# Performance work log

Measured on AMD Instinct MI355X. Metric: run time of the kernel, lower is better.

Reference implementation:

```python
import jax, jax.numpy as jnp
import numpy as np

N_NODES = 100000
N_EDGES = 1600000
N_FEAT = 32
HIDDEN = 128
N_GRAPHS = 256
NUM_LAYERS = 2
LN_EPS = 1e-5


def setup_inputs() -> dict:
    key = jax.random.key(0)
    ks = jax.random.split(key, 10)
    x = jax.random.normal(ks[0], (N_NODES, N_FEAT), dtype=jnp.float32)
    edge_index = jax.random.randint(ks[1], (2, N_EDGES), 0, N_NODES, dtype=jnp.int64)
    batch_operator = jnp.sort(jax.random.randint(ks[2], (N_NODES,), 0, N_GRAPHS, dtype=jnp.int64))
    s_in = 1.0 / np.sqrt(N_FEAT)
    s_h = 1.0 / np.sqrt(HIDDEN)
    return {
        "x": x,
        "edge_index": edge_index,
        "batch_operator": batch_operator,
        "W_op": jax.random.normal(ks[3], (N_FEAT, HIDDEN), dtype=jnp.float32) * s_in,
        "b_op": jnp.zeros((HIDDEN,), dtype=jnp.float32),
        "W_l": jax.random.normal(ks[4], (HIDDEN, HIDDEN), dtype=jnp.float32) * s_h,
        "b_l": jnp.zeros((HIDDEN,), dtype=jnp.float32),
        "W_r": jax.random.normal(ks[5], (HIDDEN, HIDDEN), dtype=jnp.float32) * s_h,
        "gamma": jnp.ones((HIDDEN,), dtype=jnp.float32),
        "beta": jnp.zeros((HIDDEN,), dtype=jnp.float32),
        "W_mem": jax.random.normal(ks[6], (HIDDEN, 1), dtype=jnp.float32) * s_h,
        "b_mem": jnp.zeros((1,), dtype=jnp.float32),
        "W_time": jax.random.normal(ks[7], (HIDDEN, 1), dtype=jnp.float32) * s_h,
        "b_time": jnp.zeros((1,), dtype=jnp.float32),
    }


def _layer_norm(h, gamma, beta):
    mu = jnp.mean(h, axis=-1, keepdims=True)
    var = jnp.mean(jnp.square(h - mu), axis=-1, keepdims=True)
    return (h - mu) * jax.lax.rsqrt(var + LN_EPS) * gamma + beta


def reference(x, edge_index, batch_operator, W_op, b_op, W_l, b_l, W_r,
              gamma, beta, W_mem, b_mem, W_time, b_time):
    src, dst = edge_index[0], edge_index[1]
    n = x.shape[0]
    # input projection
    h = x @ W_op + b_op  # [N, H]
    # scatter-mean degree (constant across layers)
    deg = jax.ops.segment_sum(jnp.ones_like(dst, dtype=h.dtype), dst, num_segments=n)
    inv_deg = 1.0 / jnp.maximum(deg, 1.0)  # [N]
    for _ in range(NUM_LAYERS):
        # SAGEConv: mean-aggregate neighbor messages, then lin_l(agg) + lin_r(root)
        agg = jax.ops.segment_sum(h[src], dst, num_segments=n) * inv_deg[:, None]
        h = agg @ W_l + b_l + h @ W_r
        h = jax.nn.elu(h)
        h = _layer_norm(h, gamma, beta)
        # dropout: identity in eval mode
    # global mean pool over graphs
    gsum = jax.ops.segment_sum(h, batch_operator, num_segments=N_GRAPHS)
    gcount = jax.ops.segment_sum(jnp.ones((n,), dtype=h.dtype), batch_operator, num_segments=N_GRAPHS)
    pooled = gsum / jnp.maximum(gcount, 1.0)[:, None]  # [B, H]
    mem_pred = (pooled @ W_mem + b_mem).squeeze(-1)
    time_pred = (pooled @ W_time + b_time).squeeze(-1)
    return (mem_pred, time_pred)
```

## Files before the change

### kernel.cpp

```cpp
#include <hip/hip_runtime.h>
#include <hip/hip_bf16.h>
#include <math.h>

#define N_NODES 100000
#define N_EDGES 1600000
#define N_FEAT 32
#define HIDDEN 128
#define N_GRAPHS 256
#define LN_EPS 1e-5f
#define NBLK_SCAN ((N_NODES + 255) / 256)

#define BSHIFT 10
#define BUCKN (1 << BSHIFT)
#define NBUCK 98
#define EPB 3840
#define NBIN ((N_EDGES + EPB - 1) / EPB)

#define LBM 128
#define AT_STRIDE 40

typedef __attribute__((ext_vector_type(8))) short bf16x8;
typedef __attribute__((ext_vector_type(4))) float f32x4;

__device__ __forceinline__ float bf2f(unsigned short u) {
    return __uint_as_float(((unsigned int)u) << 16);
}
__device__ __forceinline__ unsigned short f2bf(float f) {
    unsigned int u = __float_as_uint(f);
    u += 0x7FFFu + ((u >> 16) & 1u);
    return (unsigned short)(u >> 16);
}

__global__ __launch_bounds__(256) void scan_block_sums(const int* __restrict__ degi,
                                                       int* __restrict__ bsum) {
    __shared__ int red[256];
    int t = threadIdx.x;
    int i = blockIdx.x * 256 + t;
    red[t] = (i < N_NODES) ? degi[i] : 0;
    __syncthreads();
    #pragma unroll
    for (int off = 128; off > 0; off >>= 1) {
        if (t < off) red[t] += red[t + off];
        __syncthreads();
    }
    if (t == 0) bsum[blockIdx.x] = red[0];
}

__global__ __launch_bounds__(512) void scan_partials(const int* __restrict__ bsum,
                                                     int* __restrict__ boff) {
    __shared__ int s[512];
    int t = threadIdx.x;
    int v = (t < NBLK_SCAN) ? bsum[t] : 0;
    s[t] = v;
    __syncthreads();
    for (int off = 1; off < 512; off <<= 1) {
        int x = s[t];
        if (t >= off) x += s[t - off];
        __syncthreads();
        s[t] = x;
        __syncthreads();
    }
    if (t < NBLK_SCAN) boff[t] = s[t] - v;
}

__global__ __launch_bounds__(256) void scan_final(const int* __restrict__ degi,
                                                  const int* __restrict__ boff,
                                                  int* __restrict__ offsets,
                                                  int* __restrict__ cursor) {
    __shared__ int s[256];
    int t = threadIdx.x;
    int i = blockIdx.x * 256 + t;
    int v = (i < N_NODES) ? degi[i] : 0;
    s[t] = v;
    __syncthreads();
    for (int off = 1; off < 256; off <<= 1) {
        int x = s[t];
        if (t >= off) x += s[t - off];
        __syncthreads();
        s[t] = x;
        __syncthreads();
    }
    if (i < N_NODES) {
        int ex = s[t] - v + boff[blockIdx.x];
        offsets[i] = ex;
        cursor[i] = ex;
    }
}

__global__ __launch_bounds__(256) void hist_bucket(const int* __restrict__ dst,
                                                   int* __restrict__ histg) {
    __shared__ int h[NBUCK];
    int t = threadIdx.x;
    if (t < NBUCK) h[t] = 0;
    __syncthreads();
    int base = blockIdx.x * EPB;
    #pragma unroll
    for (int i = 0; i < EPB / 256; ++i) {
        int e = base + i * 256 + t;
        if (e < N_EDGES) atomicAdd(&h[dst[e] >> BSHIFT], 1);
    }
    __syncthreads();
    if (t < NBUCK && h[t]) atomicAdd(&histg[t], h[t]);
}

__global__ __launch_bounds__(128) void scan_bucket(const int* __restrict__ histg,
                                                   int* __restrict__ bbase,
                                                   int* __restrict__ bcur) {
    __shared__ int sb[128];
    int t = threadIdx.x;
    int v = (t < NBUCK) ? histg[t] : 0;
    sb[t] = v;
    __syncthreads();
    for (int off = 1; off < 128; off <<= 1) {
        int x = sb[t];
        if (t >= off) x += sb[t - off];
        __syncthreads();
        sb[t] = x;
        __syncthreads();
    }
    if (t < NBUCK) { bbase[t] = sb[t] - v; bcur[t] = sb[t] - v; }
    if (t == NBUCK - 1) bbase[NBUCK] = sb[t];
}

__global__ __launch_bounds__(256) void bin_pass(const int* __restrict__ src,
                                                const int* __restrict__ dst,
                                                int* __restrict__ bcur,
                                                uint2* __restrict__ stash) {
    __shared__ int srcL[EPB];
    __shared__ int dstL[EPB];
    __shared__ int hist[NBUCK], lex[NBUCK], lcur[NBUCK], gbase[NBUCK];
    __shared__ int sb[128];
    int t = threadIdx.x;
    if (t < NBUCK) hist[t] = 0;
    __syncthreads();
    int base = blockIdx.x * EPB;
    #pragma unroll
    for (int i = 0; i < EPB / 256; ++i) {
        int e = base + i * 256 + t;
        if (e < N_EDGES) atomicAdd(&hist[dst[e] >> BSHIFT], 1);
    }
    __syncthreads();
    {
        int v = (t < NBUCK) ? hist[t] : 0;
        if (t < 128) sb[t] = v;
        __syncthreads();
        for (int off = 1; off < 128; off <<= 1) {
            int x = 0;
            if (t < 128) { x = sb[t]; if (t >= off) x += sb[t - off]; }
            __syncthreads();
            if (t < 128) sb[t] = x;
            __syncthreads();
        }
        if (t < NBUCK) {
            int ex = sb[t] - hist[t];
            lex[t] = ex; lcur[t] = ex;
            gbase[t] = atomicAdd(&bcur[t], hist[t]);
        }
    }
    __syncthreads();
    #pragma unroll
    for (int i = 0; i < EPB / 256; ++i) {
        int e = base + i * 256 + t;
        if (e < N_EDGES) {
            int d = dst[e];
            int p = atomicAdd(&lcur[d >> BSHIFT], 1);
            dstL[p] = d; srcL[p] = src[e];
        }
    }
    __syncthreads();
    int n_e = min(EPB, N_EDGES - base);
    #pragma unroll
    for (int i = 0; i < EPB / 256; ++i) {
        int idx = i * 256 + t;
        if (idx < n_e) {
            int lo = 0, hi = NBUCK - 1;
            while (lo < hi) { int mid = (lo + hi + 1) >> 1; if (lex[mid] <= idx) lo = mid; else hi = mid - 1; }
            int g = gbase[lo] + (idx - lex[lo]);
            stash[g] = make_uint2((unsigned)dstL[idx], (unsigned)srcL[idx]);
        }
    }
}

__global__ __launch_bounds__(256) void deg_local(const uint2* __restrict__ stash,
                                                 const int* __restrict__ bbase,
                                                 int* __restrict__ degi) {
    __shared__ int cnt[BUCKN];
    int k = blockIdx.x;
    int t = threadIdx.x;
    #pragma unroll
    for (int i = 0; i < BUCKN / 256; ++i) cnt[i * 256 + t] = 0;
    __syncthreads();
    int beg = bbase[k], end = bbase[k + 1];
    for (int i = beg + t; i < end; i += 256)
        atomicAdd(&cnt[stash[i].x & (BUCKN - 1)], 1);
    __syncthreads();
    int nb = k << BSHIFT;
    #pragma unroll
    for (int i = 0; i < BUCKN / 256; ++i) {
        int node = nb + i * 256 + t;
        if (node < N_NODES) degi[node] = cnt[i * 256 + t];
    }
}

__global__ __launch_bounds__(256) void fill_pass(const uint2* __restrict__ stash,
                                                 const int* __restrict__ bbase,
                                                 int* __restrict__ cursor,
                                                 int* __restrict__ csr) {
    int k = blockIdx.x;
    int beg = bbase[k], end = bbase[k + 1];
    for (int i = beg + threadIdx.x; i < end; i += 256) {
        uint2 p = stash[i];
        int pos = atomicAdd(&cursor[p.x], 1);
        csr[pos] = (int)p.y;
    }
}

__global__ __launch_bounds__(256) void prep_w(const float* __restrict__ Wl,
                                              const float* __restrict__ Wr,
                                              unsigned short* __restrict__ Wt) {
    int idx = blockIdx.x * 256 + threadIdx.x;
    if (idx < HIDDEN * 2 * HIDDEN) {
        int n = idx >> 8, k = idx & 255;
        float v = (k < HIDDEN) ? Wl[k * HIDDEN + n] : Wr[(k - HIDDEN) * HIDDEN + n];
        Wt[n * 256 + k] = f2bf(v);
    }
}

__global__ __launch_bounds__(256) void proj_kernel(const float* __restrict__ x,
                                                   const float* __restrict__ W,
                                                   const float* __restrict__ b,
                                                   unsigned short* __restrict__ hb) {
    __shared__ float ws[N_FEAT][HIDDEN];
    __shared__ float bs[HIDDEN];
    __shared__ float xs[64][N_FEAT];
    int t = threadIdx.x;
    #pragma unroll
    for (int i = 0; i < 4; ++i)
        ((float4*)&ws[0][0])[t + i * 256] = ((const float4*)W)[t + i * 256];
    if (t < 32) ((float4*)bs)[t] = ((const float4*)b)[t];
    int base = blockIdx.x * 64;
    #pragma unroll
    for (int i = 0; i < 2; ++i) {
        int f4 = t + i * 256;
        int node = base + (f4 >> 3);
        float4 v = make_float4(0.f, 0.f, 0.f, 0.f);
        if (node < N_NODES) v = ((const float4*)x)[(size_t)node * 8 + (f4 & 7)];
        ((float4*)&xs[0][0])[f4] = v;
    }
    __syncthreads();
    int c0 = (t & 31) * 4;
    int nslot = t >> 5;
    for (int it = 0; it < 8; ++it) {
        int nl = nslot + it * 8;
        int node = base + nl;
        float acc0 = bs[c0], acc1 = bs[c0 + 1], acc2 = bs[c0 + 2], acc3 = bs[c0 + 3];
        #pragma unroll
        for (int k = 0; k < N_FEAT; ++k) {
            float a = xs[nl][k];
            float4 w = *(const float4*)&ws[k][c0];
            acc0 += a * w.x; acc1 += a * w.y; acc2 += a * w.z; acc3 += a * w.w;
        }
        if (node < N_NODES) {
            ushort4 o;
            o.x = f2bf(acc0); o.y = f2bf(acc1); o.z = f2bf(acc2); o.w = f2bf(acc3);
            *(ushort4*)&hb[(size_t)node * HIDDEN + c0] = o;
        }
    }
}

__global__ __launch_bounds__(256) void gather_kernel(const unsigned short* __restrict__ hb,
                                                     const int* __restrict__ csr,
                                                     const int* __restrict__ offsets,
                                                     const int* __restrict__ cursor_end,
                                                     unsigned short* __restrict__ aggb) {
    int node = (int)(((size_t)blockIdx.x * blockDim.x + threadIdx.x) >> 5);
    int lane = threadIdx.x & 31;
    if (node >= N_NODES) return;
    int st = offsets[node];
    int en = cursor_end[node];
    int dn = en - st;
    float a0[4] = {0.f, 0.f, 0.f, 0.f};
    float a1[4] = {0.f, 0.f, 0.f, 0.f};
    float a2[4] = {0.f, 0.f, 0.f, 0.f};
    float a3[4] = {0.f, 0.f, 0.f, 0.f};
    int i = st;
    for (; i + 4 <= en; i += 4) {
        int s0 = csr[i], s1 = csr[i + 1], s2 = csr[i + 2], s3 = csr[i + 3];
        ushort4 v0 = *(const ushort4*)(hb + (size_t)s0 * HIDDEN + lane * 4);
        ushort4 v1 = *(const ushort4*)(hb + (size_t)s1 * HIDDEN + lane * 4);
        ushort4 v2 = *(const ushort4*)(hb + (size_t)s2 * HIDDEN + lane * 4);
        ushort4 v3 = *(const ushort4*)(hb + (size_t)s3 * HIDDEN + lane * 4);
        a0[0] += bf2f(v0.x); a0[1] += bf2f(v0.y); a0[2] += bf2f(v0.z); a0[3] += bf2f(v0.w);
        a1[0] += bf2f(v1.x); a1[1] += bf2f(v1.y); a1[2] += bf2f(v1.z); a1[3] += bf2f(v1.w);
        a2[0] += bf2f(v2.x); a2[1] += bf2f(v2.y); a2[2] += bf2f(v2.z); a2[3] += bf2f(v2.w);
        a3[0] += bf2f(v3.x); a3[1] += bf2f(v3.y); a3[2] += bf2f(v3.z); a3[3] += bf2f(v3.w);
    }
    for (; i < en; ++i) {
        int s0 = csr[i];
        ushort4 v0 = *(const ushort4*)(hb + (size_t)s0 * HIDDEN + lane * 4);
        a0[0] += bf2f(v0.x); a0[1] += bf2f(v0.y); a0[2] += bf2f(v0.z); a0[3] += bf2f(v0.w);
    }
    float inv = 1.0f / fmaxf((float)dn, 1.0f);
    ushort4 r;
    r.x = f2bf(((a0[0] + a1[0]) + (a2[0] + a3[0])) * inv);
    r.y = f2bf(((a0[1] + a1[1]) + (a2[1] + a3[1])) * inv);
    r.z = f2bf(((a0[2] + a1[2]) + (a2[2] + a3[2])) * inv);
    r.w = f2bf(((a0[3] + a1[3]) + (a2[3] + a3[3])) * inv);
    *(ushort4*)(aggb + (size_t)node * HIDDEN + lane * 4) = r;
}

__global__ __launch_bounds__(256) void layer_mfma(const unsigned short* __restrict__ aggb,
                                                  const unsigned short* __restrict__ Wt,
                                                  const float* __restrict__ b_l,
                                                  const float* __restrict__ gamma_,
                                                  const float* __restrict__ beta_,
                                                  unsigned short* __restrict__ hb) {
    __shared__ unsigned short At[LBM * AT_STRIDE];
    int t = threadIdx.x;
    int row0 = blockIdx.x * LBM;
    int w = t >> 6;
    int l = t & 63;
    int c = l & 15;
    int g = l >> 4;
    f32x4 acc[2][8];
    #pragma unroll
    for (int fr = 0; fr < 2; ++fr)
        #pragma unroll
        for (int nf = 0; nf < 8; ++nf)
            acc[fr][nf] = (f32x4){0.f, 0.f, 0.f, 0.f};

    for (int kt = 0; kt < 8; ++kt) {
        const unsigned short* Asrc = (kt < 4) ? aggb : hb;
        int kb = (kt & 3) * 32;
        __syncthreads();
        #pragma unroll
        for (int i = 0; i < 2; ++i) {
            int ch = i * 256 + t;
            int row = ch >> 2, cc = ch & 3;
            int node = row0 + row;
            uint4 v = make_uint4(0u, 0u, 0u, 0u);
            if (node < N_NODES)
                v = *(const uint4*)(Asrc + (size_t)node * HIDDEN + kb + cc * 8);
            *(uint4*)&At[row * AT_STRIDE + cc * 8] = v;
        }
        __syncthreads();
        bf16x8 a0 = *(const bf16x8*)&At[(w * 32 + c) * AT_STRIDE + g * 8];
        bf16x8 a1 = *(const bf16x8*)&At[(w * 32 + 16 + c) * AT_STRIDE + g * 8];
        #pragma unroll
        for (int nf = 0; nf < 8; ++nf) {
            bf16x8 b = *(const bf16x8*)(Wt + (size_t)(nf * 16 + c) * 256 + kt * 32 + g * 8);
            acc[0][nf] = __builtin_amdgcn_mfma_f32_16x16x32_bf16(a0, b, acc[0][nf], 0, 0, 0);
            acc[1][nf] = __builtin_amdgcn_mfma_f32_16x16x32_bf16(a1, b, acc[1][nf], 0, 0, 0);
        }
    }
    float bl[8], ga[8], be[8];
    #pragma unroll
    for (int nf = 0; nf < 8; ++nf) {
        int col = nf * 16 + c;
        bl[nf] = b_l[col]; ga[nf] = gamma_[col]; be[nf] = beta_[col];
    }
    const float inv128 = 1.0f / 128.0f;
    #pragma unroll
    for (int fr = 0; fr < 2; ++fr) {
        #pragma unroll
        for (int r = 0; r < 4; ++r) {
            int node = row0 + w * 32 + fr * 16 + g * 4 + r;
            float v[8];
            float s = 0.f, sq = 0.f;
            #pragma unroll
            for (int nf = 0; nf < 8; ++nf) {
                float xv = acc[fr][nf][r] + bl[nf];
                xv = (xv > 0.f) ? xv : expm1f(xv);
                v[nf] = xv; s += xv; sq += xv * xv;
            }
            #pragma unroll
            for (int m = 8; m >= 1; m >>= 1) {
                s += __shfl_xor(s, m, 64);
                sq += __shfl_xor(sq, m, 64);
            }
            float mu = s * inv128;
            float var = sq * inv128 - mu * mu;
            float rstd = rsqrtf(var + LN_EPS);
            if (node < N_NODES) {
                #pragma unroll
                for (int nf = 0; nf < 8; ++nf)
                    hb[(size_t)node * HIDDEN + nf * 16 + c] =
                        f2bf((v[nf] - mu) * rstd * ga[nf] + be[nf]);
            }
        }
    }
}

__global__ __launch_bounds__(256) void pool_head_kernel(const unsigned short* __restrict__ hb,
                                                        const int* __restrict__ batch,
                                                        const float* __restrict__ W_mem,
                                                        const float* __restrict__ b_mem,
                                                        const float* __restrict__ W_time,
                                                        const float* __restrict__ b_time,
                                                        float* __restrict__ out) {
    __shared__ float red[8][HIDDEN];
    int g = blockIdx.x;
    int t = threadIdx.x;
    int lane = t & 31;
    int grp = t >> 5;
    int lo = 0, hi = N_NODES;
    while (lo < hi) { int mid = (lo + hi) >> 1; if (batch[mid] < g) lo = mid + 1; else hi = mid; }
    int start = lo;
    hi = N_NODES;
    while (lo < hi) { int mid = (lo + hi) >> 1; if (batch[mid] < g + 1) lo = mid + 1; else hi = mid; }
    int end = lo;
    float a0 = 0.f, a1 = 0.f, a2 = 0.f, a3 = 0.f;
    for (int n = start + grp; n < end; n += 8) {
        ushort4 v = *(const ushort4*)(hb + (size_t)n * HIDDEN + lane * 4);
        a0 += bf2f(v.x); a1 += bf2f(v.y); a2 += bf2f(v.z); a3 += bf2f(v.w);
    }
    red[grp][lane * 4 + 0] = a0; red[grp][lane * 4 + 1] = a1;
    red[grp][lane * 4 + 2] = a2; red[grp][lane * 4 + 3] = a3;
    __syncthreads();
    if (t < HIDDEN) {
        float s = 0.f;
        #pragma unroll
        for (int i = 0; i < 8; ++i) s += red[i][t];
        float ic = 1.0f / fmaxf((float)(end - start), 1.0f);
        red[0][t] = s * ic;
    }
    __syncthreads();
    if (t < 64) {
        float p0 = red[0][t], p1 = red[0][t + 64];
        float dm = p0 * W_mem[t] + p1 * W_mem[t + 64];
        float dtv = p0 * W_time[t] + p1 * W_time[t + 64];
        #pragma unroll
        for (int m = 32; m >= 1; m >>= 1) {
            dm += __shfl_xor(dm, m, 64);
            dtv += __shfl_xor(dtv, m, 64);
        }
        if (t == 0) {
            out[g] = dm + b_mem[0];
            out[N_GRAPHS + g] = dtv + b_time[0];
        }
    }
}

extern "C" void kernel_launch(void* const* d_in, const int* in_sizes, int n_in,
                              void* d_out, int out_size, void* d_ws, size_t ws_size,
                              hipStream_t stream) {
    const float* x      = (const float*)d_in[0];
    const int*   edge   = (const int*)d_in[1];
    const int*   batch  = (const int*)d_in[2];
    const float* W_op   = (const float*)d_in[3];
    const float* b_op   = (const float*)d_in[4];
    const float* W_l    = (const float*)d_in[5];
    const float* b_l    = (const float*)d_in[6];
    const float* W_r    = (const float*)d_in[7];
    const float* gamma_ = (const float*)d_in[8];
    const float* beta_  = (const float*)d_in[9];
    const float* W_mem  = (const float*)d_in[10];
    const float* b_mem  = (const float*)d_in[11];
    const float* W_time = (const float*)d_in[12];
    const float* b_time = (const float*)d_in[13];
    const int* src = edge;
    const int* dst = edge + N_EDGES;

    char* ws = (char*)d_ws;
    const size_t hb_bytes = (size_t)N_NODES * HIDDEN * sizeof(unsigned short);
    unsigned short* hb    = (unsigned short*)ws;
    unsigned short* aggb  = (unsigned short*)(ws + hb_bytes);
    char*  p       = ws + 2 * hb_bytes;
    unsigned short* Wt = (unsigned short*)p;  p += (size_t)HIDDEN * 2 * HIDDEN * 2;
    int*   degi    = (int*)p;                 p += (size_t)N_NODES * 4;
    int*   offsets = (int*)p;                 p += (size_t)N_NODES * 4;
    int*   cursor  = (int*)p;                 p += (size_t)N_NODES * 4;
    int*   csr     = (int*)p;                 p += (size_t)N_EDGES * 4;
    int*   bsum    = (int*)p;                 p += 2048;
    int*   boff    = (int*)p;                 p += 2048;
    int*   histg   = (int*)p;                 p += 512;
    int*   bbase   = (int*)p;                 p += 512;
    int*   bcur    = (int*)p;                 p += 512;
    uint2* stash   = (uint2*)aggb;

    hipMemsetAsync(histg, 0, NBUCK * sizeof(int), stream);

    hist_bucket<<<NBIN, 256, 0, stream>>>(dst, histg);
    scan_bucket<<<1, 128, 0, stream>>>(histg, bbase, bcur);
    bin_pass<<<NBIN, 256, 0, stream>>>(src, dst, bcur, stash);

    deg_local<<<NBUCK, 256, 0, stream>>>(stash, bbase, degi);

    scan_block_sums<<<NBLK_SCAN, 256, 0, stream>>>(degi, bsum);
    scan_partials<<<1, 512, 0, stream>>>(bsum, boff);
    scan_final<<<NBLK_SCAN, 256, 0, stream>>>(degi, boff, offsets, cursor);

    fill_pass<<<NBUCK, 256, 0, stream>>>(stash, bbase, cursor, csr);

    prep_w<<<128, 256, 0, stream>>>(W_l, W_r, Wt);
    proj_kernel<<<(N_NODES + 63) / 64, 256, 0, stream>>>(x, W_op, b_op, hb);

    for (int layer = 0; layer < 2; ++layer) {
        gather_kernel<<<(int)(((size_t)N_NODES * 32 + 255) / 256), 256, 0, stream>>>(
            hb, csr, offsets, cursor, aggb);
        layer_mfma<<<(N_NODES + LBM - 1) / LBM, 256, 0, stream>>>(
            aggb, Wt, b_l, gamma_, beta_, hb);
    }

    pool_head_kernel<<<N_GRAPHS, 256, 0, stream>>>(hb, batch, W_mem, b_mem, W_time, b_time, (float*)d_out);
}
```

Measured before the change: 495.4 us.

## Fuse degree count, scan and CSR fill into one per-bucket kernel

```diff
diff --git a/kernel.cpp b/kernel.cpp
--- a/kernel.cpp
+++ b/kernel.cpp
@@ -8,13 +8,13 @@
 #define HIDDEN 128
 #define N_GRAPHS 256
 #define LN_EPS 1e-5f
-#define NBLK_SCAN ((N_NODES + 255) / 256)
 
 #define BSHIFT 10
 #define BUCKN (1 << BSHIFT)
 #define NBUCK 98
 #define EPB 3840
 #define NBIN ((N_EDGES + EPB - 1) / EPB)
+#define CAP 24576
 
 #define LBM 128
 #define AT_STRIDE 40
@@ -29,62 +29,6 @@
     unsigned int u = __float_as_uint(f);
     u += 0x7FFFu + ((u >> 16) & 1u);
     return (unsigned short)(u >> 16);
-}
-
-__global__ __launch_bounds__(256) void scan_block_sums(const int* __restrict__ degi,
-                                                       int* __restrict__ bsum) {
-    __shared__ int red[256];
-    int t = threadIdx.x;
-    int i = blockIdx.x * 256 + t;
-    red[t] = (i < N_NODES) ? degi[i] : 0;
-    __syncthreads();
-    #pragma unroll
-    for (int off = 128; off > 0; off >>= 1) {
-        if (t < off) red[t] += red[t + off];
-        __syncthreads();
-    }
-    if (t == 0) bsum[blockIdx.x] = red[0];
-}
-
-__global__ __launch_bounds__(512) void scan_partials(const int* __restrict__ bsum,
-                                                     int* __restrict__ boff) {
-    __shared__ int s[512];
-    int t = threadIdx.x;
-    int v = (t < NBLK_SCAN) ? bsum[t] : 0;
-    s[t] = v;
-    __syncthreads();
-    for (int off = 1; off < 512; off <<= 1) {
-        int x = s[t];
-        if (t >= off) x += s[t - off];
-        __syncthreads();
-        s[t] = x;
-        __syncthreads();
-    }
-    if (t < NBLK_SCAN) boff[t] = s[t] - v;
-}
-
-__global__ __launch_bounds__(256) void scan_final(const int* __restrict__ degi,
-                                                  const int* __restrict__ boff,
-                                                  int* __restrict__ offsets,
-                                                  int* __restrict__ cursor) {
-    __shared__ int s[256];
-    int t = threadIdx.x;
-    int i = blockIdx.x * 256 + t;
-    int v = (i < N_NODES) ? degi[i] : 0;
-    s[t] = v;
-    __syncthreads();
-    for (int off = 1; off < 256; off <<= 1) {
-        int x = s[t];
-        if (t >= off) x += s[t - off];
-        __syncthreads();
-        s[t] = x;
-        __syncthreads();
-    }
-    if (i < N_NODES) {
-        int ex = s[t] - v + boff[blockIdx.x];
-        offsets[i] = ex;
-        cursor[i] = ex;
-    }
 }
 
 __global__ __launch_bounds__(256) void hist_bucket(const int* __restrict__ dst,
@@ -181,37 +125,63 @@
     }
 }
 
-__global__ __launch_bounds__(256) void deg_local(const uint2* __restrict__ stash,
-                                                 const int* __restrict__ bbase,
-                                                 int* __restrict__ degi) {
+__global__ __launch_bounds__(256) void csr_bucket(const uint2* __restrict__ stash,
+                                                  const int* __restrict__ bbase,
+                                                  int* __restrict__ offsets,
+                                                  int* __restrict__ ends,
+                                                  int* __restrict__ csr) {
     __shared__ int cnt[BUCKN];
+    __shared__ int ex[BUCKN];
+    __shared__ int sb[256];
+    __shared__ int srcL[CAP];
     int k = blockIdx.x;
     int t = threadIdx.x;
+    int beg = bbase[k], end = bbase[k + 1];
+    int ne = end - beg;
     #pragma unroll
     for (int i = 0; i < BUCKN / 256; ++i) cnt[i * 256 + t] = 0;
     __syncthreads();
-    int beg = bbase[k], end = bbase[k + 1];
     for (int i = beg + t; i < end; i += 256)
         atomicAdd(&cnt[stash[i].x & (BUCKN - 1)], 1);
     __syncthreads();
+    int c0 = cnt[t * 4], c1 = cnt[t * 4 + 1], c2 = cnt[t * 4 + 2], c3 = cnt[t * 4 + 3];
+    int gs = c0 + c1 + c2 + c3;
+    sb[t] = gs;
+    __syncthreads();
+    for (int off = 1; off < 256; off <<= 1) {
+        int x = sb[t];
+        if (t >= off) x += sb[t - off];
+        __syncthreads();
+        sb[t] = x;
+        __syncthreads();
+    }
+    int gbase_ = sb[t] - gs;
+    ex[t * 4]     = gbase_;
+    ex[t * 4 + 1] = gbase_ + c0;
+    ex[t * 4 + 2] = gbase_ + c0 + c1;
+    ex[t * 4 + 3] = gbase_ + c0 + c1 + c2;
+    __syncthreads();
+    #pragma unroll
+    for (int i = 0; i < BUCKN / 256; ++i) cnt[i * 256 + t] = ex[i * 256 + t];
+    __syncthreads();
+    for (int i = beg + t; i < end; i += 256) {
+        uint2 p = stash[i];
+        int pos = atomicAdd(&cnt[p.x & (BUCKN - 1)], 1);
+        if (pos < CAP) srcL[pos] = (int)p.y;
+        else csr[beg + pos] = (int)p.y;
+    }
+    __syncthreads();
+    int lim = min(ne, CAP);
+    for (int i = t; i < lim; i += 256) csr[beg + i] = srcL[i];
     int nb = k << BSHIFT;
     #pragma unroll
     for (int i = 0; i < BUCKN / 256; ++i) {
-        int node = nb + i * 256 + t;
-        if (node < N_NODES) degi[node] = cnt[i * 256 + t];
-    }
-}
-
-__global__ __launch_bounds__(256) void fill_pass(const uint2* __restrict__ stash,
-                                                 const int* __restrict__ bbase,
-                                                 int* __restrict__ cursor,
-                                                 int* __restrict__ csr) {
-    int k = blockIdx.x;
-    int beg = bbase[k], end = bbase[k + 1];
-    for (int i = beg + threadIdx.x; i < end; i += 256) {
-        uint2 p = stash[i];
-        int pos = atomicAdd(&cursor[p.x], 1);
-        csr[pos] = (int)p.y;
+        int idx = i * 256 + t;
+        int node = nb + idx;
+        if (node < N_NODES) {
+            offsets[node] = beg + ex[idx];
+            ends[node] = beg + cnt[idx];
+        }
     }
 }
 
@@ -271,13 +241,13 @@
 __global__ __launch_bounds__(256) void gather_kernel(const unsigned short* __restrict__ hb,
                                                      const int* __restrict__ csr,
                                                      const int* __restrict__ offsets,
-                                                     const int* __restrict__ cursor_end,
+                                                     const int* __restrict__ ends,
                                                      unsigned short* __restrict__ aggb) {
     int node = (int)(((size_t)blockIdx.x * blockDim.x + threadIdx.x) >> 5);
     int lane = threadIdx.x & 31;
     if (node >= N_NODES) return;
     int st = offsets[node];
-    int en = cursor_end[node];
+    int en = ends[node];
     int dn = en - st;
     float a0[4] = {0.f, 0.f, 0.f, 0.f};
     float a1[4] = {0.f, 0.f, 0.f, 0.f};
@@ -467,12 +437,9 @@
     unsigned short* aggb  = (unsigned short*)(ws + hb_bytes);
     char*  p       = ws + 2 * hb_bytes;
     unsigned short* Wt = (unsigned short*)p;  p += (size_t)HIDDEN * 2 * HIDDEN * 2;
-    int*   degi    = (int*)p;                 p += (size_t)N_NODES * 4;
     int*   offsets = (int*)p;                 p += (size_t)N_NODES * 4;
-    int*   cursor  = (int*)p;                 p += (size_t)N_NODES * 4;
+    int*   ends    = (int*)p;                 p += (size_t)N_NODES * 4;
     int*   csr     = (int*)p;                 p += (size_t)N_EDGES * 4;
-    int*   bsum    = (int*)p;                 p += 2048;
-    int*   boff    = (int*)p;                 p += 2048;
     int*   histg   = (int*)p;                 p += 512;
     int*   bbase   = (int*)p;                 p += 512;
     int*   bcur    = (int*)p;                 p += 512;
@@ -483,21 +450,14 @@
     hist_bucket<<<NBIN, 256, 0, stream>>>(dst, histg);
     scan_bucket<<<1, 128, 0, stream>>>(histg, bbase, bcur);
     bin_pass<<<NBIN, 256, 0, stream>>>(src, dst, bcur, stash);
-
-    deg_local<<<NBUCK, 256, 0, stream>>>(stash, bbase, degi);
-
-    scan_block_sums<<<NBLK_SCAN, 256, 0, stream>>>(degi, bsum);
-    scan_partials<<<1, 512, 0, stream>>>(bsum, boff);
-    scan_final<<<NBLK_SCAN, 256, 0, stream>>>(degi, boff, offsets, cursor);
-
-    fill_pass<<<NBUCK, 256, 0, stream>>>(stash, bbase, cursor, csr);
+    csr_bucket<<<NBUCK, 256, 0, stream>>>(stash, bbase, offsets, ends, csr);
 
     prep_w<<<128, 256, 0, stream>>>(W_l, W_r, Wt);
     proj_kernel<<<(N_NODES + 63) / 64, 256, 0, stream>>>(x, W_op, b_op, hb);
 
     for (int layer = 0; layer < 2; ++layer) {
         gather_kernel<<<(int)(((size_t)N_NODES * 32 + 255) / 256), 256, 0, stream>>>(
-            hb, csr, offsets, cursor, aggb);
+            hb, csr, offsets, ends, aggb);
         layer_mfma<<<(N_NODES + LBM - 1) / LBM, 256, 0, stream>>>(
             aggb, Wt, b_l, gamma_, beta_, hb);
     }
```

Result: faster. 454.2 us (-8.3%).
